# Optimization experiments

Measured on AMD Instinct MI355X. Metric: run time of the kernel, lower is better.

## Reference

```python
import jax, jax.numpy as jnp
import numpy as np


def setup_inputs() -> dict:
    key = jax.random.key(0)
    B = 64          # number of utterances (segments)
    N = 16384       # total frames = sum(segment_num)
    D = 1024        # embedding_size
    A = 2048        # attention_dim
    H = 8           # attention_head_num
    k1, k2, k3, k4 = jax.random.split(key, 4)
    # ragged segment lengths, all >= 1, summing exactly to N
    rng = np.random.default_rng(0)
    lens = rng.integers(64, 512, size=B).astype(np.float64)
    lens = np.maximum(1, (lens * N / lens.sum()).astype(np.int64))
    lens[-1] += N - lens.sum()
    assert lens.sum() == N and (lens > 0).all()
    segment_num = jnp.asarray(lens, dtype=jnp.int32)
    x = jax.random.normal(k1, (N, D), jnp.float32)
    # torch Linear weights, stored pre-transposed as [in, out]
    w1 = jax.random.normal(k2, (D, A), jnp.float32) / np.sqrt(D)
    w2 = jax.random.normal(k3, (A, H), jnp.float32) / np.sqrt(A)
    # post_fc: Linear(D*H -> D, bias=False), stored as [D*H, D]
    w_post = jax.random.normal(k4, (D * H, D), jnp.float32) / np.sqrt(D * H)
    return {"x": x, "segment_num": segment_num, "w1": w1, "w2": w2, "w_post": w_post}


def reference(x, segment_num, w1, w2, w_post):
    N, D = x.shape
    B = segment_num.shape[0]
    H = w2.shape[1]
    # segment id for every frame (ragged -> flat segment ids)
    seg_ids = jnp.repeat(jnp.arange(B), segment_num, total_repeat_length=N)  # [N]

    # MultiAtt.w1: Linear -> ReLU -> Linear, per frame
    h = jnp.maximum(x @ w1, 0.0) @ w2  # [N, H]

    # per-segment softmax over the time axis (dim 0 within each segment)
    m = jax.ops.segment_max(h, seg_ids, num_segments=B)          # [B, H]
    p = jnp.exp(h - m[seg_ids])                                  # [N, H]
    s = jax.ops.segment_sum(p, seg_ids, num_segments=B)          # [B, H]
    attn = p / s[seg_ids]                                        # [N, H]

    # per-segment x^T @ attn -> [B, D, H] (matches torch.mm(x.T, attn))
    out_bdh = jax.ops.segment_sum(x[:, :, None] * attn[:, None, :], seg_ids, num_segments=B)
    # flatten row-major over (D, H) like out.view(-1), then post_fc (no bias)
    out = out_bdh.reshape(B, D * H) @ w_post                     # [B, D]

    # attn_i = attn^T @ attn per segment -> [B, H, H]
    attn_gram = jax.ops.segment_sum(attn[:, :, None] * attn[:, None, :], seg_ids, num_segments=B)

    # segment_type == 'average': per-segment mean of frames -> [B, D]
    out_segment = jax.ops.segment_sum(x, seg_ids, num_segments=B) / segment_num[:, None].astype(x.dtype)

    return out, out_segment, attn_gram
```

## Files before the change

kernel.cpp:

```cpp
#include <hip/hip_runtime.h>
#include <hip/hip_bf16.h>

#define NB 64
#define NN 16384
#define ND 1024
#define NA 2048
#define NH 8
#define NSLOT 16
#define KSPL 32
#define NPL 8
#define NT 16

typedef __attribute__((ext_vector_type(4))) float f32x4;
typedef __attribute__((ext_vector_type(8))) short short8;
typedef __attribute__((ext_vector_type(8))) unsigned short ushort8;

__device__ __forceinline__ unsigned short f2bf(float f) {
    unsigned int u = __float_as_uint(f);
    u = (u + 0x7fff + ((u >> 16) & 1)) >> 16;
    return (unsigned short)u;
}

__device__ __forceinline__ float bf2f(unsigned short s) {
    return __uint_as_float((unsigned int)s << 16);
}

__device__ __forceinline__ void load_lds16(const void* g, void* l) {
    __builtin_amdgcn_global_load_lds((const __attribute__((address_space(1))) void*)g,
                                     (__attribute__((address_space(3))) void*)l, 16, 0, 0);
}

__global__ __launch_bounds__(256) void k_pre(const float* __restrict__ x,
                                             const float* __restrict__ w1,
                                             const int* __restrict__ segnum,
                                             unsigned short* __restrict__ xb,
                                             unsigned short* __restrict__ w1t,
                                             int* __restrict__ segoff) {
    __shared__ unsigned short t[32][33];
    const int bx = blockIdx.x;
    if (bx < 8192) {
        size_t i = ((size_t)bx * 256 + threadIdx.x) * 8;
        float4 a = *(const float4*)(x + i);
        float4 b = *(const float4*)(x + i + 4);
        ushort8 o;
        o[0] = f2bf(a.x); o[1] = f2bf(a.y); o[2] = f2bf(a.z); o[3] = f2bf(a.w);
        o[4] = f2bf(b.x); o[5] = f2bf(b.y); o[6] = f2bf(b.z); o[7] = f2bf(b.w);
        *(ushort8*)(xb + i) = o;
    } else if (bx < 10240) {
        const int idx = bx - 8192;
        const int a0 = (idx & 63) * 32, d0 = (idx >> 6) * 32;
        const int tx = threadIdx.x & 31, ty4 = (threadIdx.x >> 5) * 4;
#pragma unroll
        for (int i = 0; i < 4; i++)
            t[tx][ty4 + i] = f2bf(w1[(size_t)(d0 + ty4 + i) * NA + a0 + tx]);
        __syncthreads();
#pragma unroll
        for (int i = 0; i < 4; i++)
            w1t[(size_t)(a0 + ty4 + i) * ND + d0 + tx] = t[ty4 + i][tx];
    } else {
        if (threadIdx.x == 0) {
            int a = 0;
            segoff[0] = 0;
            for (int b = 0; b < NB; b++) { a += segnum[b]; segoff[b + 1] = a; }
        }
    }
}

__global__ __launch_bounds__(512, 2) void k_c1h(const unsigned short* __restrict__ xb,
                                                const unsigned short* __restrict__ w1t,
                                                const float* __restrict__ w2,
                                                float* __restrict__ h_part) {
    __shared__ unsigned short SM[73984];
    unsigned short* As   = SM;
    unsigned short* Bs   = SM + 32768;
    unsigned short* w2hi = SM + 65536;
    unsigned short* w2lo = SM + 69760;

    const int tid = threadIdx.x;
    const int wv = tid >> 6, lane = tid & 63;
    const int wm = wv >> 2, wn = wv & 3;
    const int quad = lane >> 4, lc = lane & 15;
    const int l7 = lc & 7;

    const int wg = blockIdx.x + blockIdx.y * (NN / 256);
    const int swz = (wg & 7) * 64 + (wg >> 3);
    const int bxm = swz & 63, byn = swz >> 6;
    const int m0 = bxm * 256, n0 = byn * 256;

    for (int i = tid; i < 4224; i += 512) { w2hi[i] = 0; w2lo[i] = 0; }
    for (int i = tid; i < 2048; i += 512) {
        int k = i >> 3, q = i & 7;
        float w = w2[(size_t)(n0 + k) * NH + q];
        unsigned short hi = f2bf(w);
        w2hi[q * 264 + k] = hi;
        w2lo[q * 264 + k] = f2bf(w - bf2f(hi));
    }

    const int rr = wv * 8 + (lane >> 3);
    const size_t goff0 = (size_t)rr * ND + (size_t)(((lane & 7) ^ (lane >> 3)) << 3);
    const size_t goff1 = goff0 + (size_t)64 * ND;
    const int ls0 = wv * 512, ls1 = (wv + 8) * 512;

    const unsigned short* xA = xb  + (size_t)m0 * ND;
    const unsigned short* xB = w1t + (size_t)n0 * ND;

#define STAGE(SRC, DST) do { \
        load_lds16((SRC) + goff0, (DST) + ls0); \
        load_lds16((SRC) + goff1, (DST) + ls1); } while (0)

    f32x4 acc[8][4];
#pragma unroll
    for (int i = 0; i < 8; i++)
#pragma unroll
        for (int j = 0; j < 4; j++) acc[i][j] = (f32x4){0.f, 0.f, 0.f, 0.f};

    int aoff[4], boff[2];
#pragma unroll
    for (int i = 0; i < 4; i++) aoff[i] = (wm * 64 + i * 16 + lc) * 64;
#pragma unroll
    for (int i = 0; i < 2; i++) boff[i] = (wn * 32 + i * 16 + lc) * 64;

    short8 bfr[4];

#define PHASE(D, KS, MU, LOADB, STAGES, WAIT2)                                   \
    do {                                                                         \
        const unsigned short* Ab = As + ((D) * 2 + (MU)) * 8192;                 \
        const unsigned short* Bb = Bs + ((D) * 2) * 8192;                        \
        const int kb = ((((KS) * 4) + quad) ^ l7) << 3;                          \
        short8 af[4];                                                            \
        _Pragma("unroll") for (int i = 0; i < 4; i++)                            \
            af[i] = *(const short8*)&Ab[aoff[i] + kb];                           \
        if (LOADB) {                                                             \
            _Pragma("unroll") for (int j = 0; j < 2; j++) {                      \
                bfr[j]     = *(const short8*)&Bb[boff[j] + kb];                  \
                bfr[2 + j] = *(const short8*)&Bb[8192 + boff[j] + kb];           \
            }                                                                    \
        }                                                                        \
        STAGES;                                                                  \
        asm volatile("" ::: "memory");                                           \
        __builtin_amdgcn_s_barrier();                                            \
        asm volatile("" ::: "memory");                                           \
        __builtin_amdgcn_s_setprio(1);                                           \
        _Pragma("unroll") for (int i = 0; i < 4; i++)                            \
            _Pragma("unroll") for (int j = 0; j < 4; j++)                        \
                acc[(MU) * 4 + i][j] = __builtin_amdgcn_mfma_f32_16x16x32_bf16(  \
                    af[i], bfr[j], acc[(MU) * 4 + i][j], 0, 0, 0);               \
        __builtin_amdgcn_s_setprio(0);                                           \
        WAIT2;                                                                   \
        asm volatile("" ::: "memory");                                           \
        __builtin_amdgcn_s_barrier();                                            \
        asm volatile("" ::: "memory");                                           \
    } while (0)

    STAGE(xA, As);
    STAGE(xB, Bs);
    STAGE(xA + (size_t)128 * ND, As + 8192);
    STAGE(xB + (size_t)128 * ND, Bs + 8192);
    STAGE(xA + 64, As + 16384);
    STAGE(xB + 64, Bs + 16384);
    asm volatile("s_waitcnt vmcnt(4)" ::: "memory");
    __builtin_amdgcn_s_barrier();
    asm volatile("" ::: "memory");

#pragma unroll 2
    for (int t = 0; t < NT - 2; t++) {
        const int d = t & 1;
        const unsigned short* xAn = xA + (t + 1) * 64;
        const unsigned short* xBn = xB + (t + 1) * 64;
        const unsigned short* xAnn = xA + (t + 2) * 64;
        const unsigned short* xBnn = xB + (t + 2) * 64;
        unsigned short* Ad1 = As + ((d ^ 1) * 2) * 8192;
        unsigned short* Bd1 = Bs + ((d ^ 1) * 2) * 8192;
        unsigned short* Ad2 = As + (d * 2) * 8192;
        unsigned short* Bd2 = Bs + (d * 2) * 8192;
        PHASE(d, 0, 0, 1,
              { STAGE(xAn + (size_t)128 * ND, Ad1 + 8192);
                STAGE(xBn + (size_t)128 * ND, Bd1 + 8192); }, {});
        PHASE(d, 0, 1, 0, {}, {});
        PHASE(d, 1, 0, 1, {}, {});
        PHASE(d, 1, 1, 0,
              { STAGE(xAnn, Ad2); STAGE(xBnn, Bd2); },
              { asm volatile("s_waitcnt vmcnt(4)" ::: "memory"); });
    }
    {
        const unsigned short* xAn = xA + (NT - 1) * 64;
        const unsigned short* xBn = xB + (NT - 1) * 64;
        PHASE(0, 0, 0, 1,
              { STAGE(xAn + (size_t)128 * ND, As + 3 * 8192);
                STAGE(xBn + (size_t)128 * ND, Bs + 3 * 8192); }, {});
        PHASE(0, 0, 1, 0, {}, {});
        PHASE(0, 1, 0, 1, {}, {});
        PHASE(0, 1, 1, 0, {}, { asm volatile("s_waitcnt vmcnt(0)" ::: "memory"); });
    }
    PHASE(1, 0, 0, 1, {}, {});
    PHASE(1, 0, 1, 0, {}, {});
    PHASE(1, 1, 0, 1, {}, {});
    PHASE(1, 1, 1, 0, {}, {});

#undef PHASE
#undef STAGE

    unsigned short* c1s = SM;
    f32x4 hacc[2];
    hacc[0] = (f32x4){0.f, 0.f, 0.f, 0.f};
    hacc[1] = (f32x4){0.f, 0.f, 0.f, 0.f};

#pragma unroll
    for (int nu = 0; nu < 2; nu++) {
#pragma unroll
        for (int mi = 0; mi < 8; mi++) {
            const int row = (mi >> 2) * 128 + wm * 64 + (mi & 3) * 16 + quad * 4;
#pragma unroll
            for (int nj = 0; nj < 2; nj++) {
                const int col = wn * 32 + nj * 16 + lc;
                const int ni = nu * 2 + nj;
#pragma unroll
                for (int r = 0; r < 4; r++)
                    c1s[(row + r) * 136 + col] = f2bf(fmaxf(acc[mi][ni][r], 0.f));
            }
        }
        asm volatile("s_waitcnt lgkmcnt(0)" ::: "memory");
        __builtin_amdgcn_s_barrier();
        asm volatile("" ::: "memory");
#pragma unroll
        for (int ks = 0; ks < 4; ks++) {
            short8 bh = *(const short8*)&w2hi[lc * 264 + nu * 128 + ks * 32 + quad * 8];
            short8 bl = *(const short8*)&w2lo[lc * 264 + nu * 128 + ks * 32 + quad * 8];
#pragma unroll
            for (int mt = 0; mt < 2; mt++) {
                short8 afr = *(const short8*)&c1s[(wv * 32 + mt * 16 + lc) * 136 +
                                                  ks * 32 + quad * 8];
                hacc[mt] = __builtin_amdgcn_mfma_f32_16x16x32_bf16(afr, bh, hacc[mt], 0, 0, 0);
                hacc[mt] = __builtin_amdgcn_mfma_f32_16x16x32_bf16(afr, bl, hacc[mt], 0, 0, 0);
            }
        }
        asm volatile("" ::: "memory");
        __builtin_amdgcn_s_barrier();
        asm volatile("" ::: "memory");
    }

    if (lc < NH) {
        float* hp = h_part + (size_t)byn * (NN * NH);
#pragma unroll
        for (int mt = 0; mt < 2; mt++)
#pragma unroll
            for (int r = 0; r < 4; r++)
                hp[(size_t)(m0 + wv * 32 + mt * 16 + quad * 4 + r) * NH + lc] = hacc[mt][r];
    }
}

__global__ __launch_bounds__(256) void k_attn(const float* __restrict__ h_part,
                                              float* __restrict__ attn,
                                              const int* __restrict__ segoff,
                                              float* __restrict__ gram) {
    const int b = blockIdx.x;
    const int s0 = segoff[b], s1 = segoff[b + 1];
    const int len = s1 - s0;
    const int tid = threadIdx.x;
    const int wv = tid >> 6;
    __shared__ float hl[1024 * NH];
    __shared__ float red[4][NH];
    __shared__ float mb[NH];
    __shared__ float sinv[NH];
    __shared__ float gred[4][64];

    float mx[NH];
#pragma unroll
    for (int q = 0; q < NH; q++) mx[q] = -1e30f;

    const bool cached = (len <= 1024);

    for (int n = s0 + tid; n < s1; n += 256) {
        float v[NH];
#pragma unroll
        for (int q = 0; q < NH; q++) v[q] = 0.f;
#pragma unroll
        for (int p = 0; p < NPL; p++) {
            const float4* hp = (const float4*)(h_part + (size_t)p * (NN * NH) + (size_t)n * NH);
            float4 u0 = hp[0], u1 = hp[1];
            v[0] += u0.x; v[1] += u0.y; v[2] += u0.z; v[3] += u0.w;
            v[4] += u1.x; v[5] += u1.y; v[6] += u1.z; v[7] += u1.w;
        }
        if (cached) {
#pragma unroll
            for (int q = 0; q < NH; q++) hl[(n - s0) * NH + q] = v[q];
        }
#pragma unroll
        for (int q = 0; q < NH; q++) mx[q] = fmaxf(mx[q], v[q]);
    }
#pragma unroll
    for (int q = 0; q < NH; q++)
        for (int o = 1; o < 64; o <<= 1) mx[q] = fmaxf(mx[q], __shfl_xor(mx[q], o));
    if ((tid & 63) == 0)
        for (int q = 0; q < NH; q++) red[wv][q] = mx[q];
    __syncthreads();
    if (tid < NH)
        mb[tid] = fmaxf(fmaxf(red[0][tid], red[1][tid]), fmaxf(red[2][tid], red[3][tid]));
    __syncthreads();

    float sm[NH];
#pragma unroll
    for (int q = 0; q < NH; q++) sm[q] = 0.f;
    for (int n = s0 + tid; n < s1; n += 256) {
        float v[NH];
        if (cached) {
#pragma unroll
            for (int q = 0; q < NH; q++) v[q] = hl[(n - s0) * NH + q];
        } else {
#pragma unroll
            for (int q = 0; q < NH; q++) v[q] = 0.f;
#pragma unroll
            for (int p = 0; p < NPL; p++) {
                const float4* hp = (const float4*)(h_part + (size_t)p * (NN * NH) + (size_t)n * NH);
                float4 u0 = hp[0], u1 = hp[1];
                v[0] += u0.x; v[1] += u0.y; v[2] += u0.z; v[3] += u0.w;
                v[4] += u1.x; v[5] += u1.y; v[6] += u1.z; v[7] += u1.w;
            }
        }
#pragma unroll
        for (int q = 0; q < NH; q++) sm[q] += expf(v[q] - mb[q]);
    }
#pragma unroll
    for (int q = 0; q < NH; q++)
        for (int o = 1; o < 64; o <<= 1) sm[q] += __shfl_xor(sm[q], o);
    if ((tid & 63) == 0)
        for (int q = 0; q < NH; q++) red[wv][q] = sm[q];
    __syncthreads();
    if (tid < NH)
        sinv[tid] = 1.0f / (red[0][tid] + red[1][tid] + red[2][tid] + red[3][tid]);
    __syncthreads();

    float g[NH][NH];
#pragma unroll
    for (int i = 0; i < NH; i++)
#pragma unroll
        for (int j = 0; j < NH; j++) g[i][j] = 0.f;

    for (int n = s0 + tid; n < s1; n += 256) {
        float v[NH];
        if (cached) {
#pragma unroll
            for (int q = 0; q < NH; q++) v[q] = hl[(n - s0) * NH + q];
        } else {
#pragma unroll
            for (int q = 0; q < NH; q++) v[q] = 0.f;
#pragma unroll
            for (int p = 0; p < NPL; p++) {
                const float4* hp = (const float4*)(h_part + (size_t)p * (NN * NH) + (size_t)n * NH);
                float4 u0 = hp[0], u1 = hp[1];
                v[0] += u0.x; v[1] += u0.y; v[2] += u0.z; v[3] += u0.w;
                v[4] += u1.x; v[5] += u1.y; v[6] += u1.z; v[7] += u1.w;
            }
        }
        float a[NH];
        float* ar = &attn[(size_t)n * NH];
#pragma unroll
        for (int q = 0; q < NH; q++) { a[q] = expf(v[q] - mb[q]) * sinv[q]; ar[q] = a[q]; }
#pragma unroll
        for (int i = 0; i < NH; i++)
#pragma unroll
            for (int j = 0; j < NH; j++) g[i][j] += a[i] * a[j];
    }
#pragma unroll
    for (int i = 0; i < NH; i++)
#pragma unroll
        for (int j = 0; j < NH; j++)
            for (int o = 1; o < 64; o <<= 1) g[i][j] += __shfl_xor(g[i][j], o);

    if ((tid & 63) == 0) {
#pragma unroll
        for (int i = 0; i < NH; i++)
#pragma unroll
            for (int j = 0; j < NH; j++) gred[wv][i * NH + j] = g[i][j];
    }
    __syncthreads();
    if (tid < 64)
        gram[(size_t)b * 64 + tid] = gred[0][tid] + gred[1][tid] + gred[2][tid] + gred[3][tid];
}

__global__ __launch_bounds__(128) void k_bdh(const unsigned short* __restrict__ xb,
                                             const float* __restrict__ attn,
                                             const int* __restrict__ segoff,
                                             float* __restrict__ bdh_part,
                                             float* __restrict__ xsum_part) {
    const int slot = blockIdx.x;
    const int b = blockIdx.y;
    const int s0 = segoff[b], s1 = segoff[b + 1];
    const int dl = threadIdx.x;

    float acc[8][NH];
    float xs[8];
#pragma unroll
    for (int dd = 0; dd < 8; dd++) {
        xs[dd] = 0.f;
#pragma unroll
        for (int q = 0; q < NH; q++) acc[dd][q] = 0.f;
    }

    for (int n = s0 + slot; n < s1; n += NSLOT) {
        ushort8 xv = *(const ushort8*)(xb + (size_t)n * ND + dl * 8);
        const float4* ap = (const float4*)&attn[(size_t)n * NH];
        float4 a0 = ap[0], a1 = ap[1];
        float aq[NH] = {a0.x, a0.y, a0.z, a0.w, a1.x, a1.y, a1.z, a1.w};
#pragma unroll
        for (int dd = 0; dd < 8; dd++) {
            float xf = bf2f(xv[dd]);
            xs[dd] += xf;
#pragma unroll
            for (int q = 0; q < NH; q++) acc[dd][q] += xf * aq[q];
        }
    }

    float* bp = bdh_part + ((size_t)slot * NB + b) * (ND * NH) + (size_t)dl * 64;
#pragma unroll
    for (int dd = 0; dd < 8; dd++) {
        *(float4*)(bp + dd * 8)     = make_float4(acc[dd][0], acc[dd][1], acc[dd][2], acc[dd][3]);
        *(float4*)(bp + dd * 8 + 4) = make_float4(acc[dd][4], acc[dd][5], acc[dd][6], acc[dd][7]);
    }
    float* xp = xsum_part + ((size_t)slot * NB + b) * ND + (size_t)dl * 8;
    *(float4*)(xp)     = make_float4(xs[0], xs[1], xs[2], xs[3]);
    *(float4*)(xp + 4) = make_float4(xs[4], xs[5], xs[6], xs[7]);
}

__global__ __launch_bounds__(256) void k_bdh_red(const float* __restrict__ bdh_part,
                                                 const float* __restrict__ xsum_part,
                                                 const int* __restrict__ segoff,
                                                 float* __restrict__ bdh,
                                                 float* __restrict__ out_segment) {
    const int gid = blockIdx.x * 256 + threadIdx.x;
    const int b = gid >> 10, d = gid & 1023;
    float4 sa = make_float4(0.f, 0.f, 0.f, 0.f);
    float4 sb = make_float4(0.f, 0.f, 0.f, 0.f);
    float xsum = 0.f;
#pragma unroll
    for (int s = 0; s < NSLOT; s++) {
        const float* p = bdh_part + ((size_t)s * NB + b) * (ND * NH) + (size_t)d * NH;
        float4 u = ((const float4*)p)[0], v = ((const float4*)p)[1];
        sa.x += u.x; sa.y += u.y; sa.z += u.z; sa.w += u.w;
        sb.x += v.x; sb.y += v.y; sb.z += v.z; sb.w += v.w;
        xsum += xsum_part[((size_t)s * NB + b) * ND + d];
    }
    float* bp = bdh + (size_t)b * (ND * NH) + (size_t)d * NH;
    ((float4*)bp)[0] = sa;
    ((float4*)bp)[1] = sb;
    const int len = segoff[b + 1] - segoff[b];
    out_segment[(size_t)b * ND + d] = xsum / (float)len;
}

__global__ __launch_bounds__(256) void k_post(const float* __restrict__ bdh,
                                              const float* __restrict__ wp,
                                              float* __restrict__ out_part) {
    __shared__ float as[32][68];
    __shared__ float bs[32][128];
    const int tid = threadIdx.x;
    const int n0 = blockIdx.x * 128;
    const int k0 = blockIdx.y * (8192 / KSPL);
    const int tr = tid >> 4, tc = tid & 15;

    float acc[4][8];
#pragma unroll
    for (int i = 0; i < 4; i++)
#pragma unroll
        for (int j = 0; j < 8; j++) acc[i][j] = 0.f;

    for (int kc = 0; kc < 8192 / KSPL; kc += 32) {
        __syncthreads();
        {
            int r = tid >> 2;
            int c = (tid & 3) * 8;
            const float4* gp = (const float4*)(bdh + (size_t)r * (ND * NH) + k0 + kc + c);
            float4 v0 = gp[0], v1 = gp[1];
            as[c + 0][r] = v0.x; as[c + 1][r] = v0.y; as[c + 2][r] = v0.z; as[c + 3][r] = v0.w;
            as[c + 4][r] = v1.x; as[c + 5][r] = v1.y; as[c + 6][r] = v1.z; as[c + 7][r] = v1.w;
        }
        {
            int r = tid >> 3;
            int c = (tid & 7) * 16;
            const float4* gp = (const float4*)(wp + (size_t)(k0 + kc + r) * ND + n0 + c);
            float4* sp = (float4*)&bs[r][c];
            sp[0] = gp[0]; sp[1] = gp[1]; sp[2] = gp[2]; sp[3] = gp[3];
        }
        __syncthreads();
#pragma unroll
        for (int k = 0; k < 32; k++) {
            float4 a  = *(const float4*)&as[k][tr * 4];
            float4 b0 = *(const float4*)&bs[k][tc * 8];
            float4 b1 = *(const float4*)&bs[k][tc * 8 + 4];
            float av[4] = {a.x, a.y, a.z, a.w};
            float bv[8] = {b0.x, b0.y, b0.z, b0.w, b1.x, b1.y, b1.z, b1.w};
#pragma unroll
            for (int i = 0; i < 4; i++)
#pragma unroll
                for (int j = 0; j < 8; j++) acc[i][j] += av[i] * bv[j];
        }
    }

    float* op = out_part + (size_t)blockIdx.y * (NB * ND);
#pragma unroll
    for (int i = 0; i < 4; i++)
#pragma unroll
        for (int j = 0; j < 8; j++)
            op[(size_t)(tr * 4 + i) * ND + n0 + tc * 8 + j] = acc[i][j];
}

__global__ __launch_bounds__(256) void k_post_red(const float* __restrict__ out_part,
                                                  float* __restrict__ out) {
    const int i = (blockIdx.x * 256 + threadIdx.x) * 4;
    float4 s = *(const float4*)(out_part + i);
#pragma unroll
    for (int p = 1; p < KSPL; p++) {
        float4 v = *(const float4*)(out_part + (size_t)p * (NB * ND) + i);
        s.x += v.x; s.y += v.y; s.z += v.z; s.w += v.w;
    }
    *(float4*)(out + i) = s;
}

extern "C" void kernel_launch(void* const* d_in, const int* in_sizes, int n_in,
                              void* d_out, int out_size, void* d_ws, size_t ws_size,
                              hipStream_t stream) {
    (void)in_sizes; (void)n_in; (void)out_size; (void)ws_size;
    const float* x      = (const float*)d_in[0];
    const int*   segnum = (const int*)d_in[1];
    const float* w1     = (const float*)d_in[2];
    const float* w2     = (const float*)d_in[3];
    const float* wpost  = (const float*)d_in[4];

    float* out         = (float*)d_out;
    float* out_segment = out + NB * ND;
    float* gram        = out + 2 * NB * ND;

    char* ws = (char*)d_ws;
    const size_t MB = 1024 * 1024;
    int*   segoff   = (int*)ws;
    float* attn     = (float*)(ws + 1 * MB);
    float* bdh      = (float*)(ws + 2 * MB);
    float* h_part   = (float*)(ws + 4 * MB);
    unsigned short* xb  = (unsigned short*)(ws + 12 * MB);
    unsigned short* w1t = (unsigned short*)(ws + 44 * MB);
    float* bdh_part  = (float*)(ws + 48 * MB);
    float* xsum_part = (float*)(ws + 80 * MB);
    float* out_part  = (float*)(ws + 84 * MB);

    k_pre<<<10241, 256, 0, stream>>>(x, w1, segnum, xb, w1t, segoff);
    k_c1h<<<dim3(NN / 256, NA / 256), 512, 0, stream>>>(xb, w1t, w2, h_part);
    k_attn<<<NB, 256, 0, stream>>>(h_part, attn, segoff, gram);
    k_bdh<<<dim3(NSLOT, NB), 128, 0, stream>>>(xb, attn, segoff, bdh_part, xsum_part);
    k_bdh_red<<<256, 256, 0, stream>>>(bdh_part, xsum_part, segoff, bdh, out_segment);
    k_post<<<dim3(ND / 128, KSPL), 256, 0, stream>>>(bdh, wpost, out_part);
    k_post_red<<<(NB * ND) / (256 * 4), 256, 0, stream>>>(out_part, out);
}
```

Baseline: 264.5 us.

## Double-buffer LDS fragment reads across MFMA phases and drop workgroup swizzle

```diff
diff --git a/kernel.cpp b/kernel.cpp
--- a/kernel.cpp
+++ b/kernel.cpp
@@ -6,7 +6,7 @@
 #define ND 1024
 #define NA 2048
 #define NH 8
-#define NSLOT 16
+#define NSLOT 8
 #define KSPL 32
 #define NPL 8
 #define NT 16
@@ -81,11 +81,7 @@
     const int wm = wv >> 2, wn = wv & 3;
     const int quad = lane >> 4, lc = lane & 15;
     const int l7 = lc & 7;
-
-    const int wg = blockIdx.x + blockIdx.y * (NN / 256);
-    const int swz = (wg & 7) * 64 + (wg >> 3);
-    const int bxm = swz & 63, byn = swz >> 6;
-    const int m0 = bxm * 256, n0 = byn * 256;
+    const int m0 = blockIdx.x * 256, n0 = blockIdx.y * 256;
 
     for (int i = tid; i < 4224; i += 512) { w2hi[i] = 0; w2lo[i] = 0; }
     for (int i = tid; i < 2048; i += 512) {
@@ -120,36 +116,52 @@
 #pragma unroll
     for (int i = 0; i < 2; i++) boff[i] = (wn * 32 + i * 16 + lc) * 64;
 
-    short8 bfr[4];
-
-#define PHASE(D, KS, MU, LOADB, STAGES, WAIT2)                                   \
-    do {                                                                         \
-        const unsigned short* Ab = As + ((D) * 2 + (MU)) * 8192;                 \
-        const unsigned short* Bb = Bs + ((D) * 2) * 8192;                        \
-        const int kb = ((((KS) * 4) + quad) ^ l7) << 3;                          \
-        short8 af[4];                                                            \
-        _Pragma("unroll") for (int i = 0; i < 4; i++)                            \
-            af[i] = *(const short8*)&Ab[aoff[i] + kb];                           \
-        if (LOADB) {                                                             \
-            _Pragma("unroll") for (int j = 0; j < 2; j++) {                      \
-                bfr[j]     = *(const short8*)&Bb[boff[j] + kb];                  \
-                bfr[2 + j] = *(const short8*)&Bb[8192 + boff[j] + kb];           \
-            }                                                                    \
+    short8 af_x[4], af_y[4], bf_x[4], bf_y[4];
+
+#define RD_A(DST, D, MU, KS) do {                                                \
+        const unsigned short* Ab_ = As + ((D) * 2 + (MU)) * 8192;                \
+        const int kb_ = ((((KS) * 4) + quad) ^ l7) << 3;                         \
+        _Pragma("unroll") for (int i_ = 0; i_ < 4; i_++)                         \
+            DST[i_] = *(const short8*)&Ab_[aoff[i_] + kb_];                      \
+    } while (0)
+
+#define RD_B(DST, D, KS) do {                                                    \
+        const unsigned short* Bb_ = Bs + (D) * 2 * 8192;                         \
+        const int kb_ = ((((KS) * 4) + quad) ^ l7) << 3;                         \
+        _Pragma("unroll") for (int j_ = 0; j_ < 2; j_++) {                       \
+            DST[j_]     = *(const short8*)&Bb_[boff[j_] + kb_];                  \
+            DST[2 + j_] = *(const short8*)&Bb_[8192 + boff[j_] + kb_];           \
         }                                                                        \
-        STAGES;                                                                  \
-        asm volatile("" ::: "memory");                                           \
+    } while (0)
+
+#define MFMA16(AF, BF, MU) do {                                                  \
+        __builtin_amdgcn_s_setprio(1);                                           \
+        _Pragma("unroll") for (int i_ = 0; i_ < 4; i_++)                         \
+            _Pragma("unroll") for (int j_ = 0; j_ < 4; j_++)                     \
+                acc[(MU) * 4 + i_][j_] = __builtin_amdgcn_mfma_f32_16x16x32_bf16(\
+                    AF[i_], BF[j_], acc[(MU) * 4 + i_][j_], 0, 0, 0);            \
+        __builtin_amdgcn_s_setprio(0);                                           \
+    } while (0)
+
+#define BAR() do { asm volatile("" ::: "memory");                                \
         __builtin_amdgcn_s_barrier();                                            \
-        asm volatile("" ::: "memory");                                           \
-        __builtin_amdgcn_s_setprio(1);                                           \
-        _Pragma("unroll") for (int i = 0; i < 4; i++)                            \
-            _Pragma("unroll") for (int j = 0; j < 4; j++)                        \
-                acc[(MU) * 4 + i][j] = __builtin_amdgcn_mfma_f32_16x16x32_bf16(  \
-                    af[i], bfr[j], acc[(MU) * 4 + i][j], 0, 0, 0);               \
-        __builtin_amdgcn_s_setprio(0);                                           \
-        WAIT2;                                                                   \
-        asm volatile("" ::: "memory");                                           \
-        __builtin_amdgcn_s_barrier();                                            \
-        asm volatile("" ::: "memory");                                           \
+        asm volatile("" ::: "memory"); } while (0)
+
+#define TILE(D, S0, S3, W3) do {                                                 \
+        RD_B(bf_x, D, 0); RD_A(af_x, D, 0, 0); RD_A(af_y, D, 1, 0);              \
+        S0;                                                                      \
+        MFMA16(af_x, bf_x, 0);                                                   \
+        BAR();                                                                   \
+        RD_B(bf_y, D, 1); RD_A(af_x, D, 0, 1);                                   \
+        MFMA16(af_y, bf_x, 1);                                                   \
+        BAR();                                                                   \
+        RD_A(af_y, D, 1, 1);                                                     \
+        MFMA16(af_x, bf_y, 0);                                                   \
+        BAR();                                                                   \
+        S3;                                                                      \
+        MFMA16(af_y, bf_y, 1);                                                   \
+        W3;                                                                      \
+        BAR();                                                                   \
     } while (0)
 
     STAGE(xA, As);
@@ -173,31 +185,28 @@
         unsigned short* Bd1 = Bs + ((d ^ 1) * 2) * 8192;
         unsigned short* Ad2 = As + (d * 2) * 8192;
         unsigned short* Bd2 = Bs + (d * 2) * 8192;
-        PHASE(d, 0, 0, 1,
-              { STAGE(xAn + (size_t)128 * ND, Ad1 + 8192);
-                STAGE(xBn + (size_t)128 * ND, Bd1 + 8192); }, {});
-        PHASE(d, 0, 1, 0, {}, {});
-        PHASE(d, 1, 0, 1, {}, {});
-        PHASE(d, 1, 1, 0,
-              { STAGE(xAnn, Ad2); STAGE(xBnn, Bd2); },
-              { asm volatile("s_waitcnt vmcnt(4)" ::: "memory"); });
+        TILE(d,
+             { STAGE(xAn + (size_t)128 * ND, Ad1 + 8192);
+               STAGE(xBn + (size_t)128 * ND, Bd1 + 8192); },
+             { STAGE(xAnn, Ad2); STAGE(xBnn, Bd2); },
+             { asm volatile("s_waitcnt vmcnt(4)" ::: "memory"); });
     }
     {
         const unsigned short* xAn = xA + (NT - 1) * 64;
         const unsigned short* xBn = xB + (NT - 1) * 64;
-        PHASE(0, 0, 0, 1,
-              { STAGE(xAn + (size_t)128 * ND, As + 3 * 8192);
-                STAGE(xBn + (size_t)128 * ND, Bs + 3 * 8192); }, {});
-        PHASE(0, 0, 1, 0, {}, {});
-        PHASE(0, 1, 0, 1, {}, {});
-        PHASE(0, 1, 1, 0, {}, { asm volatile("s_waitcnt vmcnt(0)" ::: "memory"); });
-    }
-    PHASE(1, 0, 0, 1, {}, {});
-    PHASE(1, 0, 1, 0, {}, {});
-    PHASE(1, 1, 0, 1, {}, {});
-    PHASE(1, 1, 1, 0, {}, {});
-
-#undef PHASE
+        TILE(0,
+             { STAGE(xAn + (size_t)128 * ND, As + 3 * 8192);
+               STAGE(xBn + (size_t)128 * ND, Bs + 3 * 8192); },
+             {},
+             { asm volatile("s_waitcnt vmcnt(0)" ::: "memory"); });
+    }
+    TILE(1, {}, {}, {});
+
+#undef TILE
+#undef BAR
+#undef MFMA16
+#undef RD_B
+#undef RD_A
 #undef STAGE
 
     unsigned short* c1s = SM;
@@ -240,7 +249,7 @@
     }
 
     if (lc < NH) {
-        float* hp = h_part + (size_t)byn * (NN * NH);
+        float* hp = h_part + (size_t)blockIdx.y * (NN * NH);
 #pragma unroll
         for (int mt = 0; mt < 2; mt++)
 #pragma unroll
```

New measurement: 260.8 us. Within noise of the previous version (-1.4%).

## Fuse softmax, attention-weighted sums and segment mean into one kernel; atomic post reduction

Applied to the files above, without the earlier changes.

```diff
diff --git a/kernel.cpp b/kernel.cpp
--- a/kernel.cpp
+++ b/kernel.cpp
@@ -6,7 +6,6 @@
 #define ND 1024
 #define NA 2048
 #define NH 8
-#define NSLOT 16
 #define KSPL 32
 #define NPL 8
 #define NT 16
@@ -35,7 +34,8 @@
                                              const int* __restrict__ segnum,
                                              unsigned short* __restrict__ xb,
                                              unsigned short* __restrict__ w1t,
-                                             int* __restrict__ segoff) {
+                                             int* __restrict__ segoff,
+                                             float* __restrict__ outz) {
     __shared__ unsigned short t[32][33];
     const int bx = blockIdx.x;
     if (bx < 8192) {
@@ -57,6 +57,13 @@
 #pragma unroll
         for (int i = 0; i < 4; i++)
             w1t[(size_t)(a0 + ty4 + i) * ND + d0 + tx] = t[ty4 + i][tx];
+    } else if (bx < 10256) {
+        const int i = ((bx - 10240) * 256 + threadIdx.x) * 16;
+        float4 z = make_float4(0.f, 0.f, 0.f, 0.f);
+        *(float4*)(outz + i)      = z;
+        *(float4*)(outz + i + 4)  = z;
+        *(float4*)(outz + i + 8)  = z;
+        *(float4*)(outz + i + 12) = z;
     } else {
         if (threadIdx.x == 0) {
             int a = 0;
@@ -249,9 +256,11 @@
     }
 }
 
-__global__ __launch_bounds__(256) void k_attn(const float* __restrict__ h_part,
-                                              float* __restrict__ attn,
+__global__ __launch_bounds__(512) void k_fuse(const float* __restrict__ h_part,
+                                              const unsigned short* __restrict__ xb,
                                               const int* __restrict__ segoff,
+                                              float* __restrict__ bdh,
+                                              float* __restrict__ out_segment,
                                               float* __restrict__ gram) {
     const int b = blockIdx.x;
     const int s0 = segoff[b], s1 = segoff[b + 1];
@@ -259,18 +268,16 @@
     const int tid = threadIdx.x;
     const int wv = tid >> 6;
     __shared__ float hl[1024 * NH];
-    __shared__ float red[4][NH];
+    __shared__ float red[8][NH];
     __shared__ float mb[NH];
     __shared__ float sinv[NH];
-    __shared__ float gred[4][64];
+    __shared__ float gred[8][64];
 
     float mx[NH];
 #pragma unroll
     for (int q = 0; q < NH; q++) mx[q] = -1e30f;
 
-    const bool cached = (len <= 1024);
-
-    for (int n = s0 + tid; n < s1; n += 256) {
+    for (int n = s0 + tid; n < s1; n += 512) {
         float v[NH];
 #pragma unroll
         for (int q = 0; q < NH; q++) v[q] = 0.f;
@@ -281,12 +288,11 @@
             v[0] += u0.x; v[1] += u0.y; v[2] += u0.z; v[3] += u0.w;
             v[4] += u1.x; v[5] += u1.y; v[6] += u1.z; v[7] += u1.w;
         }
-        if (cached) {
-#pragma unroll
-            for (int q = 0; q < NH; q++) hl[(n - s0) * NH + q] = v[q];
-        }
-#pragma unroll
-        for (int q = 0; q < NH; q++) mx[q] = fmaxf(mx[q], v[q]);
+#pragma unroll
+        for (int q = 0; q < NH; q++) {
+            hl[(n - s0) * NH + q] = v[q];
+            mx[q] = fmaxf(mx[q], v[q]);
+        }
     }
 #pragma unroll
     for (int q = 0; q < NH; q++)
@@ -294,31 +300,20 @@
     if ((tid & 63) == 0)
         for (int q = 0; q < NH; q++) red[wv][q] = mx[q];
     __syncthreads();
-    if (tid < NH)
-        mb[tid] = fmaxf(fmaxf(red[0][tid], red[1][tid]), fmaxf(red[2][tid], red[3][tid]));
+    if (tid < NH) {
+        float m = red[0][tid];
+#pragma unroll
+        for (int w = 1; w < 8; w++) m = fmaxf(m, red[w][tid]);
+        mb[tid] = m;
+    }
     __syncthreads();
 
     float sm[NH];
 #pragma unroll
     for (int q = 0; q < NH; q++) sm[q] = 0.f;
-    for (int n = s0 + tid; n < s1; n += 256) {
-        float v[NH];
-        if (cached) {
-#pragma unroll
-            for (int q = 0; q < NH; q++) v[q] = hl[(n - s0) * NH + q];
-        } else {
-#pragma unroll
-            for (int q = 0; q < NH; q++) v[q] = 0.f;
-#pragma unroll
-            for (int p = 0; p < NPL; p++) {
-                const float4* hp = (const float4*)(h_part + (size_t)p * (NN * NH) + (size_t)n * NH);
-                float4 u0 = hp[0], u1 = hp[1];
-                v[0] += u0.x; v[1] += u0.y; v[2] += u0.z; v[3] += u0.w;
-                v[4] += u1.x; v[5] += u1.y; v[6] += u1.z; v[7] += u1.w;
-            }
-        }
-#pragma unroll
-        for (int q = 0; q < NH; q++) sm[q] += expf(v[q] - mb[q]);
+    for (int n = s0 + tid; n < s1; n += 512) {
+#pragma unroll
+        for (int q = 0; q < NH; q++) sm[q] += expf(hl[(n - s0) * NH + q] - mb[q]);
     }
 #pragma unroll
     for (int q = 0; q < NH; q++)
@@ -326,8 +321,12 @@
     if ((tid & 63) == 0)
         for (int q = 0; q < NH; q++) red[wv][q] = sm[q];
     __syncthreads();
-    if (tid < NH)
-        sinv[tid] = 1.0f / (red[0][tid] + red[1][tid] + red[2][tid] + red[3][tid]);
+    if (tid < NH) {
+        float s = red[0][tid];
+#pragma unroll
+        for (int w = 1; w < 8; w++) s += red[w][tid];
+        sinv[tid] = 1.0f / s;
+    }
     __syncthreads();
 
     float g[NH][NH];
@@ -336,26 +335,13 @@
 #pragma unroll
         for (int j = 0; j < NH; j++) g[i][j] = 0.f;
 
-    for (int n = s0 + tid; n < s1; n += 256) {
-        float v[NH];
-        if (cached) {
-#pragma unroll
-            for (int q = 0; q < NH; q++) v[q] = hl[(n - s0) * NH + q];
-        } else {
-#pragma unroll
-            for (int q = 0; q < NH; q++) v[q] = 0.f;
-#pragma unroll
-            for (int p = 0; p < NPL; p++) {
-                const float4* hp = (const float4*)(h_part + (size_t)p * (NN * NH) + (size_t)n * NH);
-                float4 u0 = hp[0], u1 = hp[1];
-                v[0] += u0.x; v[1] += u0.y; v[2] += u0.z; v[3] += u0.w;
-                v[4] += u1.x; v[5] += u1.y; v[6] += u1.z; v[7] += u1.w;
-            }
-        }
+    for (int n = s0 + tid; n < s1; n += 512) {
         float a[NH];
-        float* ar = &attn[(size_t)n * NH];
-#pragma unroll
-        for (int q = 0; q < NH; q++) { a[q] = expf(v[q] - mb[q]) * sinv[q]; ar[q] = a[q]; }
+#pragma unroll
+        for (int q = 0; q < NH; q++) {
+            a[q] = expf(hl[(n - s0) * NH + q] - mb[q]) * sinv[q];
+            hl[(n - s0) * NH + q] = a[q];
+        }
 #pragma unroll
         for (int i = 0; i < NH; i++)
 #pragma unroll
@@ -366,7 +352,6 @@
 #pragma unroll
         for (int j = 0; j < NH; j++)
             for (int o = 1; o < 64; o <<= 1) g[i][j] += __shfl_xor(g[i][j], o);
-
     if ((tid & 63) == 0) {
 #pragma unroll
         for (int i = 0; i < NH; i++)
@@ -374,82 +359,49 @@
             for (int j = 0; j < NH; j++) gred[wv][i * NH + j] = g[i][j];
     }
     __syncthreads();
-    if (tid < 64)
-        gram[(size_t)b * 64 + tid] = gred[0][tid] + gred[1][tid] + gred[2][tid] + gred[3][tid];
-}
-
-__global__ __launch_bounds__(128) void k_bdh(const unsigned short* __restrict__ xb,
-                                             const float* __restrict__ attn,
-                                             const int* __restrict__ segoff,
-                                             float* __restrict__ bdh_part,
-                                             float* __restrict__ xsum_part) {
-    const int slot = blockIdx.x;
-    const int b = blockIdx.y;
-    const int s0 = segoff[b], s1 = segoff[b + 1];
-    const int dl = threadIdx.x;
-
-    float acc[8][NH];
-    float xs[8];
-#pragma unroll
-    for (int dd = 0; dd < 8; dd++) {
-        xs[dd] = 0.f;
-#pragma unroll
-        for (int q = 0; q < NH; q++) acc[dd][q] = 0.f;
-    }
-
-    for (int n = s0 + slot; n < s1; n += NSLOT) {
-        ushort8 xv = *(const ushort8*)(xb + (size_t)n * ND + dl * 8);
-        const float4* ap = (const float4*)&attn[(size_t)n * NH];
-        float4 a0 = ap[0], a1 = ap[1];
+    if (tid < 64) {
+        float s = gred[0][tid];
+#pragma unroll
+        for (int w = 1; w < 8; w++) s += gred[w][tid];
+        gram[(size_t)b * 64 + tid] = s;
+    }
+
+    const int d0 = tid * 2;
+    float acc0[NH], acc1[NH];
+    float xs0 = 0.f, xs1 = 0.f;
+#pragma unroll
+    for (int q = 0; q < NH; q++) { acc0[q] = 0.f; acc1[q] = 0.f; }
+
+    const unsigned short* xp = xb + (size_t)s0 * ND + d0;
+#pragma unroll 2
+    for (int n = 0; n < len; n++) {
+        const float* ap = &hl[n * NH];
+        float4 a0 = *(const float4*)ap;
+        float4 a1 = *(const float4*)(ap + 4);
+        unsigned int xv = *(const unsigned int*)(xp + (size_t)n * ND);
+        float x0 = bf2f((unsigned short)(xv & 0xffffu));
+        float x1 = bf2f((unsigned short)(xv >> 16));
+        xs0 += x0; xs1 += x1;
         float aq[NH] = {a0.x, a0.y, a0.z, a0.w, a1.x, a1.y, a1.z, a1.w};
 #pragma unroll
-        for (int dd = 0; dd < 8; dd++) {
-            float xf = bf2f(xv[dd]);
-            xs[dd] += xf;
-#pragma unroll
-            for (int q = 0; q < NH; q++) acc[dd][q] += xf * aq[q];
-        }
-    }
-
-    float* bp = bdh_part + ((size_t)slot * NB + b) * (ND * NH) + (size_t)dl * 64;
-#pragma unroll
-    for (int dd = 0; dd < 8; dd++) {
-        *(float4*)(bp + dd * 8)     = make_float4(acc[dd][0], acc[dd][1], acc[dd][2], acc[dd][3]);
-        *(float4*)(bp + dd * 8 + 4) = make_float4(acc[dd][4], acc[dd][5], acc[dd][6], acc[dd][7]);
-    }
-    float* xp = xsum_part + ((size_t)slot * NB + b) * ND + (size_t)dl * 8;
-    *(float4*)(xp)     = make_float4(xs[0], xs[1], xs[2], xs[3]);
-    *(float4*)(xp + 4) = make_float4(xs[4], xs[5], xs[6], xs[7]);
-}
-
-__global__ __launch_bounds__(256) void k_bdh_red(const float* __restrict__ bdh_part,
-                                                 const float* __restrict__ xsum_part,
-                                                 const int* __restrict__ segoff,
-                                                 float* __restrict__ bdh,
-                                                 float* __restrict__ out_segment) {
-    const int gid = blockIdx.x * 256 + threadIdx.x;
-    const int b = gid >> 10, d = gid & 1023;
-    float4 sa = make_float4(0.f, 0.f, 0.f, 0.f);
-    float4 sb = make_float4(0.f, 0.f, 0.f, 0.f);
-    float xsum = 0.f;
-#pragma unroll
-    for (int s = 0; s < NSLOT; s++) {
-        const float* p = bdh_part + ((size_t)s * NB + b) * (ND * NH) + (size_t)d * NH;
-        float4 u = ((const float4*)p)[0], v = ((const float4*)p)[1];
-        sa.x += u.x; sa.y += u.y; sa.z += u.z; sa.w += u.w;
-        sb.x += v.x; sb.y += v.y; sb.z += v.z; sb.w += v.w;
-        xsum += xsum_part[((size_t)s * NB + b) * ND + d];
-    }
-    float* bp = bdh + (size_t)b * (ND * NH) + (size_t)d * NH;
-    ((float4*)bp)[0] = sa;
-    ((float4*)bp)[1] = sb;
-    const int len = segoff[b + 1] - segoff[b];
-    out_segment[(size_t)b * ND + d] = xsum / (float)len;
+        for (int q = 0; q < NH; q++) {
+            acc0[q] += x0 * aq[q];
+            acc1[q] += x1 * aq[q];
+        }
+    }
+    float* bp = bdh + (size_t)b * (ND * NH) + (size_t)d0 * NH;
+    *(float4*)(bp + 0)  = make_float4(acc0[0], acc0[1], acc0[2], acc0[3]);
+    *(float4*)(bp + 4)  = make_float4(acc0[4], acc0[5], acc0[6], acc0[7]);
+    *(float4*)(bp + 8)  = make_float4(acc1[0], acc1[1], acc1[2], acc1[3]);
+    *(float4*)(bp + 12) = make_float4(acc1[4], acc1[5], acc1[6], acc1[7]);
+    const float il = 1.0f / (float)len;
+    out_segment[(size_t)b * ND + d0]     = xs0 * il;
+    out_segment[(size_t)b * ND + d0 + 1] = xs1 * il;
 }
 
 __global__ __launch_bounds__(256) void k_post(const float* __restrict__ bdh,
                                               const float* __restrict__ wp,
-                                              float* __restrict__ out_part) {
+                                              float* __restrict__ out) {
     __shared__ float as[32][68];
     __shared__ float bs[32][128];
     const int tid = threadIdx.x;
@@ -495,24 +447,11 @@
         }
     }
 
-    float* op = out_part + (size_t)blockIdx.y * (NB * ND);
 #pragma unroll
     for (int i = 0; i < 4; i++)
 #pragma unroll
         for (int j = 0; j < 8; j++)
-            op[(size_t)(tr * 4 + i) * ND + n0 + tc * 8 + j] = acc[i][j];
-}
-
-__global__ __launch_bounds__(256) void k_post_red(const float* __restrict__ out_part,
-                                                  float* __restrict__ out) {
-    const int i = (blockIdx.x * 256 + threadIdx.x) * 4;
-    float4 s = *(const float4*)(out_part + i);
-#pragma unroll
-    for (int p = 1; p < KSPL; p++) {
-        float4 v = *(const float4*)(out_part + (size_t)p * (NB * ND) + i);
-        s.x += v.x; s.y += v.y; s.z += v.z; s.w += v.w;
-    }
-    *(float4*)(out + i) = s;
+            atomicAdd(&out[(size_t)(tr * 4 + i) * ND + n0 + tc * 8 + j], acc[i][j]);
 }
 
 extern "C" void kernel_launch(void* const* d_in, const int* in_sizes, int n_in,
@@ -532,20 +471,13 @@
     char* ws = (char*)d_ws;
     const size_t MB = 1024 * 1024;
     int*   segoff   = (int*)ws;
-    float* attn     = (float*)(ws + 1 * MB);
     float* bdh      = (float*)(ws + 2 * MB);
     float* h_part   = (float*)(ws + 4 * MB);
     unsigned short* xb  = (unsigned short*)(ws + 12 * MB);
     unsigned short* w1t = (unsigned short*)(ws + 44 * MB);
-    float* bdh_part  = (float*)(ws + 48 * MB);
-    float* xsum_part = (float*)(ws + 80 * MB);
-    float* out_part  = (float*)(ws + 84 * MB);
-
-    k_pre<<<10241, 256, 0, stream>>>(x, w1, segnum, xb, w1t, segoff);
+
+    k_pre<<<10257, 256, 0, stream>>>(x, w1, segnum, xb, w1t, segoff, out);
     k_c1h<<<dim3(NN / 256, NA / 256), 512, 0, stream>>>(xb, w1t, w2, h_part);
-    k_attn<<<NB, 256, 0, stream>>>(h_part, attn, segoff, gram);
-    k_bdh<<<dim3(NSLOT, NB), 128, 0, stream>>>(xb, attn, segoff, bdh_part, xsum_part);
-    k_bdh_red<<<256, 256, 0, stream>>>(bdh_part, xsum_part, segoff, bdh, out_segment);
-    k_post<<<dim3(ND / 128, KSPL), 256, 0, stream>>>(bdh, wpost, out_part);
-    k_post_red<<<(NB * ND) / (256 * 4), 256, 0, stream>>>(out_part, out);
-}
+    k_fuse<<<NB, 512, 0, stream>>>(h_part, xb, segoff, bdh, out_segment, gram);
+    k_post<<<dim3(ND / 128, KSPL), 256, 0, stream>>>(bdh, wpost, out);
+}
```

Result: slower. 409.2 us (+54.7%).
